# Kernel tuning notes

Measured on AMD Instinct MI355X. Metric: run time of the kernel, lower is better.

## Reference

```python
import jax, jax.numpy as jnp
import numpy as np
from jax import lax

B, C, H, W = 8, 128, 48, 48
N = H * W
SPARSITY = 0.8
K_TOP = int(N * SPARSITY)


def conv2d(x, w, b, padding, dilation=1):
    # x: [B,C,H,W], w: [O,I,kh,kw]
    out = lax.conv_general_dilated(
        x, w, window_strides=(1, 1),
        padding=[(padding, padding), (padding, padding)],
        rhs_dilation=(dilation, dilation),
        dimension_numbers=('NCHW', 'OIHW', 'NCHW'))
    return out + b[None, :, None, None]


def setup_inputs() -> dict:
    key = jax.random.key(0)
    ks = jax.random.split(key, 16)
    s = 0.02
    return {
        'x': jax.random.normal(ks[0], (B, C, H, W), jnp.float32),
        'prev_features': jax.random.normal(ks[1], (B, C, H, W), jnp.float32),
        'Wq': jax.random.normal(ks[2], (C, C), jnp.float32) * s,
        'bq': jnp.zeros((C,), jnp.float32),
        'Wk': jax.random.normal(ks[3], (C, C), jnp.float32) * s,
        'bk': jnp.zeros((C,), jnp.float32),
        'Wv': jax.random.normal(ks[4], (C, C), jnp.float32) * s,
        'bv': jnp.zeros((C,), jnp.float32),
        'ref_w': jax.random.normal(ks[5], (C, C, 3, 3), jnp.float32) * s,
        'ref_b': jnp.zeros((C,), jnp.float32),
        'gate_w': jax.random.normal(ks[6], (1, C, 3, 3), jnp.float32) * s,
        'gate_b': jnp.zeros((1,), jnp.float32),
        'cov_w': jax.random.normal(ks[7], (C, C, 3, 3), jnp.float32) * s,
        'cov_b': jnp.zeros((C,), jnp.float32),
    }


def reference(x, prev_features, Wq, bq, Wk, bk, Wv, bv,
              ref_w, ref_b, gate_w, gate_b, cov_w, cov_b):
    b_, c_, h_, w_ = x.shape
    n_ = h_ * w_
    # torch x.view(B, -1, C): raw reshape of NCHW memory (NOT a transpose)
    t = x.reshape(b_, n_, c_)
    # Linear layers (torch: y = x @ W.T + b)
    Q = t @ Wq.T + bq
    Kt = (t @ Wk.T + bk).transpose(0, 2, 1)  # [B,C,N]
    V = t @ Wv.T + bv
    attn = jnp.einsum('bnc,bcm->bnm', Q, Kt) / (c_ ** 0.5)  # [B,N,N]
    # top-k masking with scatter, as in the original
    _, idx = lax.top_k(attn, K_TOP)  # [B,N,k]
    bi = jnp.arange(b_)[:, None, None]
    ni = jnp.arange(n_)[None, :, None]
    mask = jnp.zeros_like(attn).at[bi, ni, idx].set(1.0)
    attn = attn * mask - 1e10 * (1.0 - mask)
    attn = jax.nn.softmax(attn, axis=-1)
    out = jnp.einsum('bnm,bmc->bnc', attn, V)  # [B,N,C]
    # torch view([B, C, sqrt(N), sqrt(N)]): raw reshape
    xs = out.reshape(b_, c_, h_, w_)
    # localized refinement
    importance = jax.nn.sigmoid(conv2d(xs, gate_w, gate_b, padding=1))
    xr = conv2d(xs * importance, ref_w, ref_b, padding=1)
    xs = xs + xr
    # temporal propagation
    xs = xs + 0.5 * prev_features
    # fast coverage conv: kernel 3, dilation 2, padding = 1 + 2 - 1 = 2
    return conv2d(xs, cov_w, cov_b, padding=2, dilation=2)
```

## Files before the change

### kernel.cpp

```cpp
#include <hip/hip_runtime.h>
#include <hip/hip_bf16.h>
#include <math.h>

#define BB 8
#define CC 128
#define NTOK 2304
#define KTOP 1843

typedef unsigned short u16;
typedef unsigned int   u32;
typedef __attribute__((ext_vector_type(8))) short short8;
typedef __attribute__((ext_vector_type(4))) float f32x4;

static __device__ __forceinline__ float bf2f(u16 u) {
    return __uint_as_float(((u32)u) << 16);
}
static __device__ __forceinline__ u16 f2bf(float f) {
    u32 x = __float_as_uint(f);
    return (u16)((x + 0x7fffu + ((x >> 16) & 1u)) >> 16);
}
static __device__ __forceinline__ float key2val(int k) {
    u32 raw = (k & 0x8000) ? (u32)(k ^ 0x8000) : ((~(u32)k) & 0xFFFFu);
    return __uint_as_float(raw << 16);
}

__global__ __launch_bounds__(256) void qkv_kernel(
    const float* __restrict__ x,
    const float* __restrict__ Wq, const float* __restrict__ bq,
    const float* __restrict__ Wk, const float* __restrict__ bk,
    const float* __restrict__ Wv, const float* __restrict__ bv,
    u16* __restrict__ q_ws, u16* __restrict__ k_ws, u16* __restrict__ v_ws)
{
    __shared__ float t_lds[128 * 68];
    __shared__ u16 st[64 * 128];
    int blk = blockIdx.x;
    int b  = blk / 36;
    int n0 = (blk % 36) * 64;
    int tid = threadIdx.x;
    const float* xb = x + (size_t)(b * NTOK + n0) * CC;
    #pragma unroll
    for (int k = 0; k < 32; ++k) {
        int idx = k * 256 + tid;
        t_lds[(idx & 127) * 68 + (idx >> 7)] = xb[idx];
    }
    __syncthreads();
    int o  = tid & 127;
    int rh = tid >> 7;
    const float* Ws[3] = {Wq, Wk, Wv};
    const float* bs[3] = {bq, bk, bv};
    for (int mat = 0; mat < 3; ++mat) {
        const float* W = Ws[mat];
        float acc[32];
        #pragma unroll
        for (int j = 0; j < 32; ++j) acc[j] = 0.f;
        for (int c = 0; c < 128; ++c) {
            float w = W[o * 128 + c];
            const float4* t4p = (const float4*)&t_lds[c * 68 + rh * 32];
            #pragma unroll
            for (int j4 = 0; j4 < 8; ++j4) {
                float4 t4 = t4p[j4];
                acc[j4*4+0] += t4.x * w;
                acc[j4*4+1] += t4.y * w;
                acc[j4*4+2] += t4.z * w;
                acc[j4*4+3] += t4.w * w;
            }
        }
        float bias = bs[mat][o];
        if (mat == 2) {
            ushort4* vp4 = (ushort4*)(v_ws + (size_t)(b * CC + o) * NTOK + n0 + rh * 32);
            #pragma unroll
            for (int j8 = 0; j8 < 8; ++j8) {
                ushort4 s;
                s.x = f2bf(acc[j8*4+0] + bias); s.y = f2bf(acc[j8*4+1] + bias);
                s.z = f2bf(acc[j8*4+2] + bias); s.w = f2bf(acc[j8*4+3] + bias);
                vp4[j8] = s;
            }
        } else {
            float sc = (mat == 0) ? 0.08838834764831845f : 1.0f;
            #pragma unroll
            for (int j = 0; j < 32; ++j)
                st[(rh * 32 + j) * 128 + o] = f2bf((acc[j] + bias) * sc);
            __syncthreads();
            u16* gp = (mat == 0 ? q_ws : k_ws) + (size_t)(b * NTOK + n0) * CC;
            const ushort4* s4 = (const ushort4*)st;
            ushort4* g4 = (ushort4*)gp;
            for (int k = tid; k < 2048; k += 256) g4[k] = s4[k];
            __syncthreads();
        }
    }
}

__global__ __launch_bounds__(256) void qk_kernel(
    const u16* __restrict__ q_ws, const u16* __restrict__ k_ws,
    u16* __restrict__ sc)
{
    int tid = threadIdx.x;
    int lane = tid & 63, wid = tid >> 6;
    int blk = blockIdx.x;
    int b = blk & 7;
    int t = blk >> 3;
    int qt = t % 36, mt = t / 36;
    int q0 = qt * 64 + wid * 16;
    int m0 = mt * 64;
    int fr = lane & 15, fg = lane >> 4;

    const u16* qb = q_ws + (size_t)(b * NTOK + q0 + fr) * CC + fg * 8;
    short8 qa[4];
    #pragma unroll
    for (int kc = 0; kc < 4; ++kc) qa[kc] = *(const short8*)(qb + kc * 32);

    const u16* kb = k_ws + (size_t)(b * NTOK + m0 + fr) * CC + fg * 8;
    f32x4 acc[4];
    #pragma unroll
    for (int i = 0; i < 4; ++i) acc[i] = (f32x4){0.f, 0.f, 0.f, 0.f};
    #pragma unroll
    for (int mt2 = 0; mt2 < 4; ++mt2) {
        const u16* kp = kb + (size_t)(mt2 * 16) * CC;
        #pragma unroll
        for (int kc = 0; kc < 4; ++kc) {
            short8 kf = *(const short8*)(kp + kc * 32);
            acc[mt2] = __builtin_amdgcn_mfma_f32_16x16x32_bf16(qa[kc], kf, acc[mt2], 0, 0, 0);
        }
    }
    #pragma unroll
    for (int mt2 = 0; mt2 < 4; ++mt2) {
        #pragma unroll
        for (int r = 0; r < 4; ++r) {
            int row = q0 + fg * 4 + r;
            int col = m0 + mt2 * 16 + fr;
            u16 raw = f2bf(acc[mt2][r]);
            u16 key = (raw & 0x8000u) ? (u16)~raw : (u16)(raw | 0x8000u);
            sc[((size_t)b * NTOK + row) * NTOK + col] = key;
        }
    }
}

__global__ __launch_bounds__(256) void topk_kernel(
    u16* __restrict__ sc, float4* __restrict__ params)
{
    int tid = threadIdx.x;
    int lane = tid & 63, wid = tid >> 6;
    size_t rg0 = (size_t)blockIdx.x * 8 + wid * 2;
    u16* s0 = sc + rg0 * NTOK;
    u16* s1 = s0 + NTOK;

    int keys0[36], keys1[36];
    int kmax0 = 0, kmax1 = 0;
    #pragma unroll
    for (int j = 0; j < 9; ++j) {
        ushort4 a = *(const ushort4*)(s0 + j * 256 + lane * 4);
        ushort4 c = *(const ushort4*)(s1 + j * 256 + lane * 4);
        keys0[j*4+0] = a.x; keys0[j*4+1] = a.y; keys0[j*4+2] = a.z; keys0[j*4+3] = a.w;
        keys1[j*4+0] = c.x; keys1[j*4+1] = c.y; keys1[j*4+2] = c.z; keys1[j*4+3] = c.w;
        kmax0 = max(kmax0, max(max((int)a.x, (int)a.y), max((int)a.z, (int)a.w)));
        kmax1 = max(kmax1, max(max((int)c.x, (int)c.y), max((int)c.z, (int)c.w)));
    }
    #pragma unroll
    for (int off = 32; off; off >>= 1) {
        kmax0 = max(kmax0, __shfl_xor(kmax0, off, 64));
        kmax1 = max(kmax1, __shfl_xor(kmax1, off, 64));
    }
    u32 res0 = 0, res1 = 0;
    for (int bit = 15; bit >= 0; --bit) {
        int cand0 = (int)(res0 | (1u << bit));
        int cand1 = (int)(res1 | (1u << bit));
        int c0 = 0, c1 = 0;
        #pragma unroll
        for (int j = 0; j < 36; ++j) {
            c0 += (keys0[j] >= cand0) ? 1 : 0;
            c1 += (keys1[j] >= cand1) ? 1 : 0;
        }
        #pragma unroll
        for (int off = 32; off; off >>= 1) {
            c0 += __shfl_xor(c0, off, 64);
            c1 += __shfl_xor(c1, off, 64);
        }
        if (c0 >= KTOP) res0 = (u32)cand0;
        if (c1 >= KTOP) res1 = (u32)cand1;
    }
    float vmax0 = key2val(kmax0), vmax1 = key2val(kmax1);
    float sum0 = 0.f, sum1 = 0.f;
    #pragma unroll
    for (int j = 0; j < 9; ++j) {
        ushort4 w0, w1;
        float e;
        e = ((u32)keys0[j*4+0] >= res0) ? __expf(key2val(keys0[j*4+0]) - vmax0) : 0.f; sum0 += e; w0.x = f2bf(e);
        e = ((u32)keys0[j*4+1] >= res0) ? __expf(key2val(keys0[j*4+1]) - vmax0) : 0.f; sum0 += e; w0.y = f2bf(e);
        e = ((u32)keys0[j*4+2] >= res0) ? __expf(key2val(keys0[j*4+2]) - vmax0) : 0.f; sum0 += e; w0.z = f2bf(e);
        e = ((u32)keys0[j*4+3] >= res0) ? __expf(key2val(keys0[j*4+3]) - vmax0) : 0.f; sum0 += e; w0.w = f2bf(e);
        e = ((u32)keys1[j*4+0] >= res1) ? __expf(key2val(keys1[j*4+0]) - vmax1) : 0.f; sum1 += e; w1.x = f2bf(e);
        e = ((u32)keys1[j*4+1] >= res1) ? __expf(key2val(keys1[j*4+1]) - vmax1) : 0.f; sum1 += e; w1.y = f2bf(e);
        e = ((u32)keys1[j*4+2] >= res1) ? __expf(key2val(keys1[j*4+2]) - vmax1) : 0.f; sum1 += e; w1.z = f2bf(e);
        e = ((u32)keys1[j*4+3] >= res1) ? __expf(key2val(keys1[j*4+3]) - vmax1) : 0.f; sum1 += e; w1.w = f2bf(e);
        *(ushort4*)(s0 + j * 256 + lane * 4) = w0;
        *(ushort4*)(s1 + j * 256 + lane * 4) = w1;
    }
    #pragma unroll
    for (int off = 32; off; off >>= 1) {
        sum0 += __shfl_xor(sum0, off, 64);
        sum1 += __shfl_xor(sum1, off, 64);
    }
    if (lane == 0) {
        params[rg0]     = make_float4(0.f, vmax0, 1.f / sum0, 0.f);
        params[rg0 + 1] = make_float4(0.f, vmax1, 1.f / sum1, 0.f);
    }
}

__global__ __launch_bounds__(256) void pv_kernel(
    const u16* __restrict__ sc, const u16* __restrict__ v_ws,
    const float4* __restrict__ params, float* __restrict__ xs_ws)
{
    int tid = threadIdx.x;
    int lane = tid & 63, wid = tid >> 6;
    int blk = blockIdx.x;
    int b = blk & 7;
    int rt = blk >> 3;
    int r0 = rt * 16;
    int c0 = wid * 32;
    int fr = lane & 15, fg = lane >> 4;
    int row = r0 + fr;

    const u16* pb = sc + ((size_t)b * NTOK + row) * NTOK + fg * 8;
    const u16* vb = v_ws + ((size_t)b * CC + c0 + fr) * NTOK + fg * 8;

    f32x4 acc0 = {0.f, 0.f, 0.f, 0.f};
    f32x4 acc1 = {0.f, 0.f, 0.f, 0.f};

    #pragma unroll 4
    for (int ch = 0; ch < 72; ++ch) {
        int m0 = ch * 32;
        short8 pa = *(const short8*)(pb + m0);
        short8 vf0 = *(const short8*)(vb + m0);
        short8 vf1 = *(const short8*)(vb + (size_t)16 * NTOK + m0);
        acc0 = __builtin_amdgcn_mfma_f32_16x16x32_bf16(pa, vf0, acc0, 0, 0, 0);
        acc1 = __builtin_amdgcn_mfma_f32_16x16x32_bf16(pa, vf1, acc1, 0, 0, 0);
    }
    #pragma unroll
    for (int r = 0; r < 4; ++r) {
        int orow = r0 + fg * 4 + r;
        float inv = params[(size_t)b * NTOK + orow].z;
        float* op = xs_ws + ((size_t)b * NTOK + orow) * CC + c0;
        op[fr]      = acc0[r] * inv;
        op[16 + fr] = acc1[r] * inv;
    }
}

__global__ __launch_bounds__(256) void gate_kernel(
    const float* __restrict__ xs_ws, const float* __restrict__ gw,
    const float* __restrict__ gb, float* __restrict__ imp_ws)
{
    __shared__ float gsum[256];
    int blk = blockIdx.x;
    int b  = blk & 7;
    int p0 = (blk >> 3) * 64;
    int tid = threadIdx.x;
    int pl = tid & 63, cq = tid >> 6;
    int p = p0 + pl;
    int h = p / 48, w = p % 48;
    float acc = 0.f;
    const float* xb = xs_ws + (size_t)b * CC * NTOK;
    for (int i = cq * 32; i < cq * 32 + 32; ++i) {
        const float* plane = xb + (size_t)i * NTOK;
        const float* wv = gw + i * 9;
        #pragma unroll
        for (int kh = 0; kh < 3; ++kh) {
            int hh = h + kh - 1;
            if ((unsigned)hh >= 48u) continue;
            #pragma unroll
            for (int kw = 0; kw < 3; ++kw) {
                int ww = w + kw - 1;
                if ((unsigned)ww >= 48u) continue;
                acc += plane[hh * 48 + ww] * wv[kh * 3 + kw];
            }
        }
    }
    gsum[cq * 64 + pl] = acc;
    __syncthreads();
    if (tid < 64) {
        float s = gsum[tid] + gsum[64 + tid] + gsum[128 + tid] + gsum[192 + tid] + gb[0];
        imp_ws[b * NTOK + p0 + tid] = 1.f / (1.f + __expf(-s));
    }
}

__global__ __launch_bounds__(256) void wtrans_kernel(
    const float* __restrict__ rw, const float* __restrict__ cw,
    u16* __restrict__ wb_ref, u16* __restrict__ wb_cov)
{
    int idx = blockIdx.x * 256 + threadIdx.x;
    int which = idx >= 147456;
    int rem = which ? idx - 147456 : idx;
    int tap = rem >> 14;
    int rest = rem & 16383;
    int o = rest >> 7, c = rest & 127;
    const float* src = which ? cw : rw;
    u16* dst = which ? wb_cov : wb_ref;
    dst[rem] = f2bf(src[(o * 128 + c) * 9 + tap]);
}

__global__ __launch_bounds__(256) void tpos_kernel(
    const float* __restrict__ xs_ws, const float* __restrict__ prev,
    const float* __restrict__ imp_ws,
    u16* __restrict__ xt_g, float* __restrict__ rbuf)
{
    __shared__ float tx[128 * 65];
    __shared__ float tp[128 * 65];
    int blk = blockIdx.x;
    int b  = blk & 7;
    int p0 = (blk >> 3) * 64;
    int tid = threadIdx.x;
    const float* xsb = xs_ws + (size_t)b * CC * NTOK + p0;
    const float* pvb = prev  + (size_t)b * CC * NTOK + p0;
    #pragma unroll
    for (int it = 0; it < 32; ++it) {
        int idx = it * 256 + tid;
        int i = idx >> 6, pp = idx & 63;
        tx[i * 65 + pp] = xsb[(size_t)i * NTOK + pp];
        tp[i * 65 + pp] = pvb[(size_t)i * NTOK + pp];
    }
    __syncthreads();
    int pl = tid & 63, cq = tid >> 6;
    float impv = imp_ws[b * NTOK + p0 + pl];
    size_t obase = ((size_t)b * NTOK + p0 + pl) * CC + cq * 32;
    u16* gout = xt_g + obase;
    float* rout = rbuf + obase;
    #pragma unroll
    for (int j4 = 0; j4 < 8; ++j4) {
        float4 rv; ushort4 gv;
        float v0 = tx[(cq * 32 + j4 * 4 + 0) * 65 + pl];
        float v1 = tx[(cq * 32 + j4 * 4 + 1) * 65 + pl];
        float v2 = tx[(cq * 32 + j4 * 4 + 2) * 65 + pl];
        float v3 = tx[(cq * 32 + j4 * 4 + 3) * 65 + pl];
        float q0 = tp[(cq * 32 + j4 * 4 + 0) * 65 + pl];
        float q1 = tp[(cq * 32 + j4 * 4 + 1) * 65 + pl];
        float q2 = tp[(cq * 32 + j4 * 4 + 2) * 65 + pl];
        float q3 = tp[(cq * 32 + j4 * 4 + 3) * 65 + pl];
        rv.x = v0 + 0.5f * q0; rv.y = v1 + 0.5f * q1;
        rv.z = v2 + 0.5f * q2; rv.w = v3 + 0.5f * q3;
        gv.x = f2bf(v0 * impv); gv.y = f2bf(v1 * impv);
        gv.z = f2bf(v2 * impv); gv.w = f2bf(v3 * impv);
        *(float4*)(rout + j4 * 4) = rv;
        *(ushort4*)(gout + j4 * 4) = gv;
    }
}

__global__ __launch_bounds__(256) void refgemm_kernel(
    const u16* __restrict__ xt_g, const u16* __restrict__ wb_ref,
    const float* __restrict__ rbuf, const float* __restrict__ rb,
    u16* __restrict__ xt2)
{
    __shared__ u16 slab[144 * 128];
    int tid = threadIdx.x;
    int lane = tid & 63, wid = tid >> 6;
    int blk = blockIdx.x;
    int b  = blk & 7;
    int st = (blk >> 3) & 15;
    int oh = blk >> 7;
    int h0 = st * 3;
    int p0g = st * 144;
    int fr = lane & 15, fg = lane >> 4;
    int o0 = oh * 64 + wid * 16;
    const u16* xb = xt_g + (size_t)b * NTOK * CC;

    f32x4 acc[9];
    #pragma unroll
    for (int pt = 0; pt < 9; ++pt) acc[pt] = (f32x4){0.f, 0.f, 0.f, 0.f};

    for (int tap = 0; tap < 9; ++tap) {
        int dh = tap / 3 - 1, dw = tap % 3 - 1;
        __syncthreads();
        #pragma unroll
        for (int it = 0; it < 9; ++it) {
            int idx = it * 256 + tid;
            int pr = idx >> 4, cv = idx & 15;
            int r = pr >= 96 ? 2 : (pr >= 48 ? 1 : 0);
            int w = pr - r * 48;
            int sh = h0 + r + dh, sw = w + dw;
            short8 val = (short8){0,0,0,0,0,0,0,0};
            if ((unsigned)sh < 48u && (unsigned)sw < 48u)
                val = *(const short8*)(xb + (size_t)(sh * 48 + sw) * CC + cv * 8);
            *(short8*)(slab + pr * 128 + ((cv ^ (pr & 7)) * 8)) = val;
        }
        __syncthreads();
        #pragma unroll
        for (int kc = 0; kc < 4; ++kc) {
            short8 bfr = *(const short8*)(wb_ref + tap * 16384 + (o0 + fr) * 128 + kc * 32 + fg * 8);
            #pragma unroll
            for (int pt = 0; pt < 9; ++pt) {
                int prr = pt * 16 + fr;
                short8 pa = *(const short8*)(slab + prr * 128 + (((kc * 4 + fg) ^ (prr & 7)) * 8));
                acc[pt] = __builtin_amdgcn_mfma_f32_16x16x32_bf16(pa, bfr, acc[pt], 0, 0, 0);
            }
        }
    }
    int o = o0 + fr;
    float bias = rb[o];
    #pragma unroll
    for (int pt = 0; pt < 9; ++pt) {
        #pragma unroll
        for (int r = 0; r < 4; ++r) {
            int p = p0g + pt * 16 + fg * 4 + r;
            size_t off = ((size_t)b * NTOK + p) * CC + o;
            float v = acc[pt][r] + bias + rbuf[off];
            xt2[off] = f2bf(v);
        }
    }
}

__global__ __launch_bounds__(256) void covgemm_kernel(
    const u16* __restrict__ xt2, const u16* __restrict__ wb_cov,
    const float* __restrict__ cb, float* __restrict__ out)
{
    __shared__ u16 slab[144 * 128];
    __shared__ float ldsout[4 * 16 * 145];
    int tid = threadIdx.x;
    int lane = tid & 63, wid = tid >> 6;
    int blk = blockIdx.x;
    int b  = blk & 7;
    int st = (blk >> 3) & 15;
    int oh = blk >> 7;
    int h0 = st * 3;
    int p0g = st * 144;
    int fr = lane & 15, fg = lane >> 4;
    int o0 = oh * 64 + wid * 16;
    const u16* xb = xt2 + (size_t)b * NTOK * CC;

    f32x4 acc[9];
    #pragma unroll
    for (int pt = 0; pt < 9; ++pt) acc[pt] = (f32x4){0.f, 0.f, 0.f, 0.f};

    for (int tap = 0; tap < 9; ++tap) {
        int dh = (tap / 3 - 1) * 2, dw = (tap % 3 - 1) * 2;
        __syncthreads();
        #pragma unroll
        for (int it = 0; it < 9; ++it) {
            int idx = it * 256 + tid;
            int pr = idx >> 4, cv = idx & 15;
            int r = pr >= 96 ? 2 : (pr >= 48 ? 1 : 0);
            int w = pr - r * 48;
            int sh = h0 + r + dh, sw = w + dw;
            short8 val = (short8){0,0,0,0,0,0,0,0};
            if ((unsigned)sh < 48u && (unsigned)sw < 48u)
                val = *(const short8*)(xb + (size_t)(sh * 48 + sw) * CC + cv * 8);
            *(short8*)(slab + pr * 128 + ((cv ^ (pr & 7)) * 8)) = val;
        }
        __syncthreads();
        #pragma unroll
        for (int kc = 0; kc < 4; ++kc) {
            short8 bfr = *(const short8*)(wb_cov + tap * 16384 + (o0 + fr) * 128 + kc * 32 + fg * 8);
            #pragma unroll
            for (int pt = 0; pt < 9; ++pt) {
                int prr = pt * 16 + fr;
                short8 pa = *(const short8*)(slab + prr * 128 + (((kc * 4 + fg) ^ (prr & 7)) * 8));
                acc[pt] = __builtin_amdgcn_mfma_f32_16x16x32_bf16(pa, bfr, acc[pt], 0, 0, 0);
            }
        }
    }
    float bias = cb[o0 + fr];
    float* lo = ldsout + wid * (16 * 145);
    #pragma unroll
    for (int pt = 0; pt < 9; ++pt) {
        #pragma unroll
        for (int r = 0; r < 4; ++r) {
            int pl = pt * 16 + fg * 4 + r;
            lo[fr * 145 + pl] = acc[pt][r] + bias;
        }
    }
    __syncthreads();
    float* ob = out + ((size_t)b * CC + o0) * NTOK + p0g;
    #pragma unroll
    for (int j = 0; j < 36; ++j) {
        int idx = j * 64 + lane;
        int o_r = idx / 144;
        int p_r = idx - o_r * 144;
        ob[(size_t)o_r * NTOK + p_r] = lo[o_r * 145 + p_r];
    }
}

extern "C" void kernel_launch(void* const* d_in, const int* in_sizes, int n_in,
                              void* d_out, int out_size, void* d_ws, size_t ws_size,
                              hipStream_t stream)
{
    const float* x    = (const float*)d_in[0];
    const float* prev = (const float*)d_in[1];
    const float* Wq   = (const float*)d_in[2];
    const float* bq   = (const float*)d_in[3];
    const float* Wk   = (const float*)d_in[4];
    const float* bk   = (const float*)d_in[5];
    const float* Wv   = (const float*)d_in[6];
    const float* bv   = (const float*)d_in[7];
    const float* rw   = (const float*)d_in[8];
    const float* rb   = (const float*)d_in[9];
    const float* gw   = (const float*)d_in[10];
    const float* gb   = (const float*)d_in[11];
    const float* cw   = (const float*)d_in[12];
    const float* cb   = (const float*)d_in[13];
    float* out = (float*)d_out;
    char* ws = (char*)d_ws;

    const size_t SZ  = (size_t)BB * NTOK * CC;
    const size_t BSZ = SZ * 2;
    const size_t FSZ = SZ * 4;
    const size_t SCB = (size_t)BB * NTOK * NTOK * 2;
    const size_t PRB = (size_t)BB * NTOK * 16;
    const size_t RIB = (size_t)BB * NTOK * 4;

    size_t off = 0;
    u16*    q_ws   = (u16*)(ws + off);    off += BSZ;
    u16*    k_ws   = (u16*)(ws + off);    off += BSZ;
    u16*    v_ws   = (u16*)(ws + off);    off += BSZ;
    u16*    sc_ws  = (u16*)(ws + off);    off += SCB;
    float4* prm_ws = (float4*)(ws + off); off += PRB;
    float*  xs_ws  = (float*)(ws + off);  off += FSZ;
    float*  imp_ws = (float*)(ws + off);  off += RIB;
    u16*    xt_g   = (u16*)(ws + off);    off += BSZ;
    float*  rbuf   = (float*)(ws + off);  off += FSZ;
    u16*    xt2    = (u16*)(ws + off);    off += BSZ;
    u16*    wb_ref = (u16*)(ws + off);    off += 294912;
    u16*    wb_cov = (u16*)(ws + off);    off += 294912;

    qkv_kernel<<<dim3(288), dim3(256), 0, stream>>>(x, Wq, bq, Wk, bk, Wv, bv,
                                                    q_ws, k_ws, v_ws);
    qk_kernel<<<dim3(10368), dim3(256), 0, stream>>>(q_ws, k_ws, sc_ws);
    topk_kernel<<<dim3(2304), dim3(256), 0, stream>>>(sc_ws, prm_ws);
    pv_kernel<<<dim3(1152), dim3(256), 0, stream>>>(sc_ws, v_ws, prm_ws, xs_ws);
    gate_kernel<<<dim3(288), dim3(256), 0, stream>>>(xs_ws, gw, gb, imp_ws);
    wtrans_kernel<<<dim3(1152), dim3(256), 0, stream>>>(rw, cw, wb_ref, wb_cov);
    tpos_kernel<<<dim3(288), dim3(256), 0, stream>>>(xs_ws, prev, imp_ws, xt_g, rbuf);
    refgemm_kernel<<<dim3(256), dim3(256), 0, stream>>>(xt_g, wb_ref, rbuf, rb, xt2);
    covgemm_kernel<<<dim3(256), dim3(256), 0, stream>>>(xt2, wb_cov, cb, out);
}
```

Before: 574.8 us.

## Split PV reduction dimension across waves and reduce partials in LDS

The PV matmul kernel now gives each of the four waves a quarter of the token (reduction) range covering all 128 channels, instead of giving each wave 32 channels over the full range. Each wave loads its score fragment once and reuses it across eight MFMA tiles, so the block reads each score row once rather than four times. Partial results are summed through a padded shared-memory buffer before scaling and storing. This adds an LDS reduction, a block barrier and more accumulator registers per wave.

```diff
diff --git a/kernel.cpp b/kernel.cpp
--- a/kernel.cpp
+++ b/kernel.cpp
@@ -210,38 +210,61 @@
     const u16* __restrict__ sc, const u16* __restrict__ v_ws,
     const float4* __restrict__ params, float* __restrict__ xs_ws)
 {
+    __shared__ float red[4 * 16 * 130];
     int tid = threadIdx.x;
     int lane = tid & 63, wid = tid >> 6;
     int blk = blockIdx.x;
     int b = blk & 7;
     int rt = blk >> 3;
     int r0 = rt * 16;
-    int c0 = wid * 32;
     int fr = lane & 15, fg = lane >> 4;
     int row = r0 + fr;
-
-    const u16* pb = sc + ((size_t)b * NTOK + row) * NTOK + fg * 8;
-    const u16* vb = v_ws + ((size_t)b * CC + c0 + fr) * NTOK + fg * 8;
-
-    f32x4 acc0 = {0.f, 0.f, 0.f, 0.f};
-    f32x4 acc1 = {0.f, 0.f, 0.f, 0.f};
-
-    #pragma unroll 4
-    for (int ch = 0; ch < 72; ++ch) {
+    int mbase = wid * 576;
+
+    const u16* pb = sc + ((size_t)b * NTOK + row) * NTOK + mbase + fg * 8;
+    const u16* vb = v_ws + ((size_t)b * CC + fr) * NTOK + mbase + fg * 8;
+
+    f32x4 acc[8];
+    #pragma unroll
+    for (int i = 0; i < 8; ++i) acc[i] = (f32x4){0.f, 0.f, 0.f, 0.f};
+
+    #pragma unroll 2
+    for (int ch = 0; ch < 18; ++ch) {
         int m0 = ch * 32;
         short8 pa = *(const short8*)(pb + m0);
-        short8 vf0 = *(const short8*)(vb + m0);
-        short8 vf1 = *(const short8*)(vb + (size_t)16 * NTOK + m0);
-        acc0 = __builtin_amdgcn_mfma_f32_16x16x32_bf16(pa, vf0, acc0, 0, 0, 0);
-        acc1 = __builtin_amdgcn_mfma_f32_16x16x32_bf16(pa, vf1, acc1, 0, 0, 0);
-    }
-    #pragma unroll
-    for (int r = 0; r < 4; ++r) {
-        int orow = r0 + fg * 4 + r;
-        float inv = params[(size_t)b * NTOK + orow].z;
-        float* op = xs_ws + ((size_t)b * NTOK + orow) * CC + c0;
-        op[fr]      = acc0[r] * inv;
-        op[16 + fr] = acc1[r] * inv;
+        short8 vf0 = *(const short8*)(vb + (size_t)(0 * 16) * NTOK + m0);
+        short8 vf1 = *(const short8*)(vb + (size_t)(1 * 16) * NTOK + m0);
+        short8 vf2 = *(const short8*)(vb + (size_t)(2 * 16) * NTOK + m0);
+        short8 vf3 = *(const short8*)(vb + (size_t)(3 * 16) * NTOK + m0);
+        short8 vf4 = *(const short8*)(vb + (size_t)(4 * 16) * NTOK + m0);
+        short8 vf5 = *(const short8*)(vb + (size_t)(5 * 16) * NTOK + m0);
+        short8 vf6 = *(const short8*)(vb + (size_t)(6 * 16) * NTOK + m0);
+        short8 vf7 = *(const short8*)(vb + (size_t)(7 * 16) * NTOK + m0);
+        acc[0] = __builtin_amdgcn_mfma_f32_16x16x32_bf16(pa, vf0, acc[0], 0, 0, 0);
+        acc[1] = __builtin_amdgcn_mfma_f32_16x16x32_bf16(pa, vf1, acc[1], 0, 0, 0);
+        acc[2] = __builtin_amdgcn_mfma_f32_16x16x32_bf16(pa, vf2, acc[2], 0, 0, 0);
+        acc[3] = __builtin_amdgcn_mfma_f32_16x16x32_bf16(pa, vf3, acc[3], 0, 0, 0);
+        acc[4] = __builtin_amdgcn_mfma_f32_16x16x32_bf16(pa, vf4, acc[4], 0, 0, 0);
+        acc[5] = __builtin_amdgcn_mfma_f32_16x16x32_bf16(pa, vf5, acc[5], 0, 0, 0);
+        acc[6] = __builtin_amdgcn_mfma_f32_16x16x32_bf16(pa, vf6, acc[6], 0, 0, 0);
+        acc[7] = __builtin_amdgcn_mfma_f32_16x16x32_bf16(pa, vf7, acc[7], 0, 0, 0);
+    }
+    float* myred = red + wid * (16 * 130);
+    #pragma unroll
+    for (int t = 0; t < 8; ++t)
+        #pragma unroll
+        for (int r = 0; r < 4; ++r)
+            myred[(fg * 4 + r) * 130 + t * 16 + fr] = acc[t][r];
+    __syncthreads();
+    #pragma unroll
+    for (int k = 0; k < 8; ++k) {
+        int idx = k * 256 + tid;
+        int rr = idx >> 7, c = idx & 127;
+        int loff = rr * 130 + c;
+        float s = red[loff] + red[16 * 130 + loff]
+                + red[2 * 16 * 130 + loff] + red[3 * 16 * 130 + loff];
+        float inv = params[(size_t)b * NTOK + r0 + rr].z;
+        xs_ws[((size_t)b * NTOK + r0 + rr) * CC + c] = s * inv;
     }
 }
 
```

Result: faster. 543.2 us (-5.5%).
